# Performance work log

Measured on AMD Instinct MI355X. Metric: run time of the kernel, lower is better.

The kernel has to match this reference:

```python
import jax, jax.numpy as jnp
import numpy as np

N_NODES = 100000
N_RELS = 237
N_EDGES = 500000
D_IN = 128
D_HID = 128
D_OUT = 128


def setup_inputs() -> dict:
    key = jax.random.key(0)
    ks = jax.random.split(key, 13)
    src = jax.random.randint(ks[0], (N_EDGES,), 0, N_NODES, dtype=jnp.int32)
    dst = jax.random.randint(ks[1], (N_EDGES,), 0, N_NODES, dtype=jnp.int32)
    rel = jax.random.randint(ks[2], (N_EDGES,), 0, N_RELS, dtype=jnp.int32)
    triplets = jnp.stack([src, dst, rel], axis=1)  # [E, 3]
    s = 0.05
    return {
        "triplets": triplets,
        "ent_embed": jax.random.normal(ks[3], (N_NODES, D_IN), jnp.float32) * s,
        "rel_embed": jax.random.normal(ks[4], (N_RELS, D_IN), jnp.float32) * s,
        "W_ent": jax.random.normal(ks[5], (D_IN, D_HID), jnp.float32) * s,
        "b_ent": jnp.zeros((D_HID,), jnp.float32),
        "W_rel": jax.random.normal(ks[6], (D_IN, D_HID), jnp.float32) * s,
        "b_rel": jnp.zeros((D_HID,), jnp.float32),
        "W_ent2": jax.random.normal(ks[7], (3 * D_HID, D_OUT), jnp.float32) * s,
        "b_ent2": jnp.zeros((D_OUT,), jnp.float32),
        "a_w": jax.random.normal(ks[8], (D_OUT, 1), jnp.float32) * s,
        "a_b": jnp.zeros((1,), jnp.float32),
    }


def reference(triplets, ent_embed, rel_embed, W_ent, b_ent, W_rel, b_rel,
              W_ent2, b_ent2, a_w, a_b):
    src_i, dst_i, rel_i = triplets[:, 0], triplets[:, 1], triplets[:, 2]
    # embedding gathers
    src = ent_embed[src_i]          # [E, D_IN]
    dst = ent_embed[dst_i]          # [E, D_IN]
    rel = rel_embed[rel_i]          # [E, D_IN]
    # shared fc_ent projection on src and dst, fc_rel on rel
    src = src @ W_ent + b_ent       # [E, D_HID]
    dst = dst @ W_ent + b_ent
    rel = rel @ W_rel + b_rel
    # per-edge feature c = fc_ent2(cat([src, dst, rel]))
    c = jnp.concatenate([src, dst, rel], axis=1) @ W_ent2 + b_ent2  # [E, D_OUT]
    # unnormalized exp attention score (leaky_relu slope 0.01, torch default)
    b = jnp.exp(jax.nn.leaky_relu((c @ a_w + a_b)[:, 0], negative_slope=0.01))  # [E]
    # segment softmax over edges sharing a source node
    b_sum = jax.ops.segment_sum(b, src_i, num_segments=N_NODES)  # [N]
    alpha = b / b_sum[src_i]                                     # [E]
    # weighted neighbor aggregation per source node
    h = jax.ops.segment_sum(alpha[:, None] * c, src_i, num_segments=N_NODES)  # [N, D_OUT]
    return h
```

## Files before the change

### kernel.cpp

```cpp
#include <hip/hip_runtime.h>
#include <hip/hip_bf16.h>

#define N_NODES_C 100000
#define N_PAD_C   100096
#define N_RELS_C  237
#define N_EDGES_C 500000
#define D 128

#define NBLK_HIST 128
#define NBLK_REL  60
#define NBLK_GEMM 782
#define GEMM0     (NBLK_HIST + NBLK_REL)

typedef __attribute__((ext_vector_type(8))) short short8;
typedef __attribute__((ext_vector_type(4))) float f32x4;

__device__ __forceinline__ ushort f2bf(float x) {
    union { float f; uint u; } v; v.f = x;
    uint r = v.u + 0x7FFFu + ((v.u >> 16) & 1u);
    return (ushort)(r >> 16);
}
__device__ __forceinline__ float bf2f_hi(uint u) {
    union { uint u; float f; } v; v.u = u; return v.f;
}

__global__ void k_fuse_w(const float* __restrict__ W_ent, const float* __restrict__ W_rel,
                         const float* __restrict__ W_ent2,
                         const float* __restrict__ b_ent, const float* __restrict__ b_rel,
                         const float* __restrict__ b_ent2,
                         const float* __restrict__ a_w, const float* __restrict__ a_b,
                         float* __restrict__ WR, ushort* __restrict__ WfTb,
                         float* __restrict__ biasC, float* __restrict__ sConst,
                         int* __restrict__ deg) {
    int j = threadIdx.x;
    int k = blockIdx.x;
    int which = blockIdx.y;
    if (which == 0) {
        float acc = 0.f;
        for (int i = 0; i < D; ++i) acc += W_ent[k*D+i] * W_ent2[i*D+j];
        WfTb[j*D + k] = f2bf(acc);
    } else if (which == 1) {
        float acc = 0.f;
        for (int i = 0; i < D; ++i) acc += W_ent[k*D+i] * W_ent2[(D+i)*D+j];
        WfTb[(D+j)*D + k] = f2bf(acc);
    } else if (which == 2) {
        float acc = 0.f;
        for (int i = 0; i < D; ++i) acc += W_rel[k*D+i] * W_ent2[(2*D+i)*D+j];
        WR[k*D + j] = acc;
    } else if (k == 0) {
        __shared__ float red[128];
        float acc = b_ent2[j];
        for (int i = 0; i < D; ++i) {
            acc += b_ent[i] * (W_ent2[i*D+j] + W_ent2[(D+i)*D+j]);
            acc += b_rel[i] * W_ent2[(2*D+i)*D+j];
        }
        biasC[j] = acc;
        red[j] = acc * a_w[j];
        __syncthreads();
        for (int s = 64; s > 0; s >>= 1) { if (j < s) red[j] += red[j+s]; __syncthreads(); }
        if (j == 0) sConst[0] = red[0] + a_b[0];
    } else {
        int idx = (k - 1) * 128 + j;
        for (int i = idx; i < N_NODES_C; i += 127 * 128) deg[i] = 0;
    }
}

__global__ __launch_bounds__(512, 6) void k1_mega(const float* __restrict__ ent,
                                                  const ushort* __restrict__ WfTb,
                                                  const float* __restrict__ a_w,
                                                  const float* __restrict__ relE,
                                                  const float* __restrict__ WR,
                                                  const int* __restrict__ trip,
                                                  ushort* __restrict__ AnB,
                                                  ushort* __restrict__ BnB,
                                                  ushort* __restrict__ RmB,
                                                  float* __restrict__ sA,
                                                  float* __restrict__ sB,
                                                  float* __restrict__ sR,
                                                  int* __restrict__ deg,
                                                  int n_nodes) {
    __shared__ __align__(16) ushort wL[128*128];
    int tid = threadIdx.x;
    int blk = blockIdx.x;

    if (blk < NBLK_HIST) {
        for (int e = blk*512 + tid; e < N_EDGES_C; e += NBLK_HIST*512) {
            int s = trip[3*e];
            if ((unsigned)s < (unsigned)N_NODES_C) atomicAdd(&deg[s], 1);
        }
        return;
    }
    if (blk < GEMM0) {
        __shared__ float red[512];
        int sub = tid >> 7, j = tid & 127;
        int r = (blk - NBLK_HIST)*4 + sub;
        float acc = 0.f;
        if (r < N_RELS_C) {
            for (int k = 0; k < D; ++k) acc += relE[r*D+k] * WR[k*D+j];
            RmB[r*D + j] = f2bf(acc);
        }
        red[tid] = acc * a_w[j];
        __syncthreads();
        for (int s = 64; s > 0; s >>= 1) {
            if (j < s) red[sub*128 + j] += red[sub*128 + j + s];
            __syncthreads();
        }
        if (j == 0 && r < N_RELS_C) sR[r] = red[sub*128];
        return;
    }

    int tile = blk - GEMM0;
    int m0   = tile * 128;

    int wave = tid >> 6, lane = tid & 63;
    int q = lane >> 4, c = lane & 15;

    int row = m0 + wave*16 + c;
    float4 e0[4], e1[4];
#pragma unroll
    for (int chunk = 0; chunk < 4; ++chunk) {
        e0[chunk] = make_float4(0.f,0.f,0.f,0.f);
        e1[chunk] = e0[chunk];
    }
    if (row < n_nodes) {
        const float* ep = &ent[(size_t)row*D];
#pragma unroll
        for (int chunk = 0; chunk < 4; ++chunk) {
            int k16 = chunk*4 + q;
            e0[chunk] = *(const float4*)(ep + (k16 << 3));
            e1[chunk] = *(const float4*)(ep + (k16 << 3) + 4);
        }
    }

#pragma unroll
    for (int u = 0; u < 4; ++u) {
        int f = u*512 + tid;
        int r = f >> 4, k16 = f & 15;
        *(uint4*)&wL[r*128 + ((k16 ^ (r & 15)) << 3)] =
            *(const uint4*)&WfTb[r*128 + (k16 << 3)];
    }

    short8 a[4];
#pragma unroll
    for (int chunk = 0; chunk < 4; ++chunk) {
        short8 pk;
        pk[0]=(short)f2bf(e0[chunk].x); pk[1]=(short)f2bf(e0[chunk].y);
        pk[2]=(short)f2bf(e0[chunk].z); pk[3]=(short)f2bf(e0[chunk].w);
        pk[4]=(short)f2bf(e1[chunk].x); pk[5]=(short)f2bf(e1[chunk].y);
        pk[6]=(short)f2bf(e1[chunk].z); pk[7]=(short)f2bf(e1[chunk].w);
        a[chunk] = pk;
    }

    float aw[8];
#pragma unroll
    for (int nt = 0; nt < 8; ++nt) aw[nt] = a_w[nt*16 + c];

    __syncthreads();

    f32x4 acc[8];
#pragma unroll
    for (int nt = 0; nt < 8; ++nt) { f32x4 z = {0.f,0.f,0.f,0.f}; acc[nt] = z; }

#pragma unroll
    for (int chunk = 0; chunk < 4; ++chunk) {
        int k16 = chunk*4 + q;
#pragma unroll
        for (int nt = 0; nt < 8; ++nt) {
            short8 b = *(const short8*)&wL[(nt*16 + c)*128 + ((k16 ^ c) << 3)];
            acc[nt] = __builtin_amdgcn_mfma_f32_16x16x32_bf16(a[chunk], b, acc[nt], 0, 0, 0);
        }
    }

    __syncthreads();

#pragma unroll
    for (int u = 0; u < 4; ++u) {
        int f = u*512 + tid;
        int r = f >> 4, k16 = f & 15;
        *(uint4*)&wL[r*128 + ((k16 ^ (r & 15)) << 3)] =
            *(const uint4*)&WfTb[(128 + r)*128 + (k16 << 3)];
    }

#pragma unroll
    for (int reg = 0; reg < 4; ++reg) {
        int m = m0 + wave*16 + q*4 + reg;
        float pa = 0.f;
#pragma unroll
        for (int nt = 0; nt < 8; ++nt) pa += acc[nt][reg] * aw[nt];
#pragma unroll
        for (int msk = 1; msk < 16; msk <<= 1) pa += __shfl_xor(pa, msk);
        if (m < n_nodes) {
            if (c == 0) sA[m] = pa;
#pragma unroll
            for (int nt = 0; nt < 8; ++nt)
                AnB[(size_t)m*D + nt*16 + c] = f2bf(acc[nt][reg]);
        }
    }

    __syncthreads();

#pragma unroll
    for (int nt = 0; nt < 8; ++nt) { f32x4 z = {0.f,0.f,0.f,0.f}; acc[nt] = z; }

#pragma unroll
    for (int chunk = 0; chunk < 4; ++chunk) {
        int k16 = chunk*4 + q;
#pragma unroll
        for (int nt = 0; nt < 8; ++nt) {
            short8 b = *(const short8*)&wL[(nt*16 + c)*128 + ((k16 ^ c) << 3)];
            acc[nt] = __builtin_amdgcn_mfma_f32_16x16x32_bf16(a[chunk], b, acc[nt], 0, 0, 0);
        }
    }

#pragma unroll
    for (int reg = 0; reg < 4; ++reg) {
        int m = m0 + wave*16 + q*4 + reg;
        float pa = 0.f;
#pragma unroll
        for (int nt = 0; nt < 8; ++nt) pa += acc[nt][reg] * aw[nt];
#pragma unroll
        for (int msk = 1; msk < 16; msk <<= 1) pa += __shfl_xor(pa, msk);
        if (m < n_nodes) {
            if (c == 0) sB[m] = pa;
#pragma unroll
            for (int nt = 0; nt < 8; ++nt)
                BnB[(size_t)m*D + nt*16 + c] = f2bf(acc[nt][reg]);
        }
    }
}

__global__ void k_scan1(const int* __restrict__ deg, int* __restrict__ off,
                        int* __restrict__ bsum, int n) {
    __shared__ int s[1024];
    int i = blockIdx.x*1024 + threadIdx.x;
    int v = (i < n) ? deg[i] : 0;
    s[threadIdx.x] = v; __syncthreads();
    for (int d = 1; d < 1024; d <<= 1) {
        int t = (threadIdx.x >= d) ? s[threadIdx.x - d] : 0;
        __syncthreads();
        s[threadIdx.x] += t;
        __syncthreads();
    }
    if (i < n) off[i] = s[threadIdx.x] - v;
    if (threadIdx.x == 1023) bsum[blockIdx.x] = s[1023];
}

__global__ void k_scan23(int* __restrict__ off, int* __restrict__ cursor,
                         const int* __restrict__ bsum, int n, int nb, int total_edges) {
    __shared__ int s[128];
    int t = threadIdx.x;
    if (t < 128) s[t] = (t < nb) ? bsum[t] : 0;
    __syncthreads();
    for (int d = 1; d < 128; d <<= 1) {
        int u = (t < 128 && t >= d) ? s[t - d] : 0;
        __syncthreads();
        if (t < 128) s[t] += u;
        __syncthreads();
    }
    int add = (blockIdx.x > 0) ? s[blockIdx.x - 1] : 0;
    int i = blockIdx.x*1024 + t;
    if (i < n) {
        int o = off[i] + add;
        off[i] = o;
        cursor[i] = o;
    }
    if (i == 0) off[n] = total_edges;
}

__global__ void k_edge_b(const int* __restrict__ trip, const float* __restrict__ sB,
                         const float* __restrict__ sR, int* __restrict__ cursor,
                         uint2* __restrict__ kb, int n_edges) {
    int e = blockIdx.x*256 + threadIdx.x;
    if (e >= n_edges) return;
    int s = trip[3*e], d = trip[3*e+1], r = trip[3*e+2];
    if ((unsigned)s >= (unsigned)N_NODES_C || (unsigned)d >= (unsigned)N_NODES_C ||
        (unsigned)r >= (unsigned)N_RELS_C) return;
    float v = sB[d] + sR[r];
    int p = atomicAdd(&cursor[s], 1);
    kb[p] = make_uint2((uint)(d | (r << 20)), __float_as_uint(v));
}

__global__ void k_aggregate(const int* __restrict__ off, const uint2* __restrict__ kb,
                            const ushort* __restrict__ AnB, const ushort* __restrict__ BnB,
                            const ushort* __restrict__ RmB, const float* __restrict__ biasC,
                            const float* __restrict__ sA, const float* __restrict__ sConst,
                            float* __restrict__ h, int n_nodes) {
    int g = threadIdx.x >> 4, lane = threadIdx.x & 15;
    int n = blockIdx.x*16 + g;
    if (n >= n_nodes) return;
    int o0 = off[n], o1 = off[n+1];
    int c = lane*8;
    float* hp = &h[(size_t)n*D + c];
    if (o0 == o1) {
        *(float4*)hp     = make_float4(0.f,0.f,0.f,0.f);
        *(float4*)(hp+4) = make_float4(0.f,0.f,0.f,0.f);
        return;
    }
    float t = sA[n] + sConst[0];
    float num[8];
#pragma unroll
    for (int i = 0; i < 8; ++i) num[i] = 0.f;
    float den = 0.f;

    for (int p = o0; p < o1; p += 4) {
        uint2 kv[4]; uint4 gB[4], gR[4]; float vmask[4];
#pragma unroll
        for (int u = 0; u < 4; ++u) {
            int q = p + u;
            vmask[u] = (q < o1) ? 1.f : 0.f;
            int pc = (q < o1) ? q : (o1 - 1);
            kv[u] = kb[pc];
        }
#pragma unroll
        for (int u = 0; u < 4; ++u) {
            gB[u] = *(const uint4*)&BnB[(size_t)(kv[u].x & 0xFFFFF)*D + c];
            gR[u] = *(const uint4*)&RmB[(size_t)(kv[u].x >> 20)*D + c];
        }
#pragma unroll
        for (int u = 0; u < 4; ++u) {
            float logit = t + __uint_as_float(kv[u].y);
            float l = logit > 0.f ? logit : 0.01f*logit;
            float b = vmask[u] * expf(l);
            den += b;
            const uint* bu = (const uint*)&gB[u];
            const uint* ru = (const uint*)&gR[u];
#pragma unroll
            for (int i = 0; i < 4; ++i) {
                num[2*i]   += b * (bf2f_hi(bu[i] << 16)         + bf2f_hi(ru[i] << 16));
                num[2*i+1] += b * (bf2f_hi(bu[i] & 0xFFFF0000u) + bf2f_hi(ru[i] & 0xFFFF0000u));
            }
        }
    }

    float inv = 1.f / den;
    uint4 araw = *(const uint4*)&AnB[(size_t)n*D + c];
    const uint* au = (const uint*)&araw;
    float4 bc0 = *(const float4*)&biasC[c];
    float4 bc1 = *(const float4*)&biasC[c+4];
    float4 o0v, o1v;
    o0v.x = bf2f_hi(au[0] << 16)         + bc0.x + num[0]*inv;
    o0v.y = bf2f_hi(au[0] & 0xFFFF0000u) + bc0.y + num[1]*inv;
    o0v.z = bf2f_hi(au[1] << 16)         + bc0.z + num[2]*inv;
    o0v.w = bf2f_hi(au[1] & 0xFFFF0000u) + bc0.w + num[3]*inv;
    o1v.x = bf2f_hi(au[2] << 16)         + bc1.x + num[4]*inv;
    o1v.y = bf2f_hi(au[2] & 0xFFFF0000u) + bc1.y + num[5]*inv;
    o1v.z = bf2f_hi(au[3] << 16)         + bc1.z + num[6]*inv;
    o1v.w = bf2f_hi(au[3] & 0xFFFF0000u) + bc1.w + num[7]*inv;
    *(float4*)hp     = o0v;
    *(float4*)(hp+4) = o1v;
}

extern "C" void kernel_launch(void* const* d_in, const int* in_sizes, int n_in,
                              void* d_out, int out_size, void* d_ws, size_t ws_size,
                              hipStream_t stream) {
    const int*   trip   = (const int*)  d_in[0];
    const float* ent    = (const float*)d_in[1];
    const float* relE   = (const float*)d_in[2];
    const float* W_ent  = (const float*)d_in[3];
    const float* b_ent  = (const float*)d_in[4];
    const float* W_rel  = (const float*)d_in[5];
    const float* b_rel  = (const float*)d_in[6];
    const float* W_ent2 = (const float*)d_in[7];
    const float* b_ent2 = (const float*)d_in[8];
    const float* a_w    = (const float*)d_in[9];
    const float* a_b    = (const float*)d_in[10];
    float* h = (float*)d_out;

    char* ws = (char*)d_ws;
    size_t o = 0;
    auto alloc = [&](size_t bytes) { size_t p = o; o += (bytes + 255) & ~(size_t)255; return p; };
    float*  WR     = (float*) (ws + alloc(128*128*4));
    ushort* WfTb   = (ushort*)(ws + alloc(256*128*2));
    float*  biasC  = (float*) (ws + alloc(128*4));
    ushort* RmB    = (ushort*)(ws + alloc((size_t)N_RELS_C*128*2));
    float*  sR     = (float*) (ws + alloc(N_RELS_C*4));
    float*  sConst = (float*) (ws + alloc(4));
    float*  sA     = (float*) (ws + alloc((size_t)N_NODES_C*4));
    float*  sB     = (float*) (ws + alloc((size_t)N_NODES_C*4));
    int*    deg    = (int*)   (ws + alloc((size_t)N_NODES_C*4));
    int*    off    = (int*)   (ws + alloc(((size_t)N_NODES_C+1)*4));
    int*    cursor = (int*)   (ws + alloc((size_t)N_NODES_C*4));
    int*    bsum   = (int*)   (ws + alloc(128*4));
    uint2*  kb     = (uint2*) (ws + alloc((size_t)N_EDGES_C*8));
    ushort* BnB    = (ushort*)(ws + alloc((size_t)N_PAD_C*128*2));
    ushort* AnB    = (ushort*)(ws + alloc((size_t)N_PAD_C*128*2));

    k_fuse_w<<<dim3(128,4), 128, 0, stream>>>(W_ent, W_rel, W_ent2, b_ent, b_rel, b_ent2,
                                              a_w, a_b, WR, WfTb, biasC, sConst, deg);
    k1_mega<<<GEMM0 + NBLK_GEMM, 512, 0, stream>>>(
        ent, WfTb, a_w, relE, WR, trip, AnB, BnB, RmB, sA, sB, sR, deg, N_NODES_C);
    int nb = (N_NODES_C + 1023)/1024;
    k_scan1<<<nb, 1024, 0, stream>>>(deg, off, bsum, N_NODES_C);
    k_scan23<<<nb, 1024, 0, stream>>>(off, cursor, bsum, N_NODES_C, nb, N_EDGES_C);
    k_edge_b<<<(N_EDGES_C+255)/256, 256, 0, stream>>>(trip, sB, sR, cursor, kb, N_EDGES_C);
    k_aggregate<<<(N_NODES_C+15)/16, 256, 0, stream>>>(off, kb, AnB, BnB, RmB, biasC,
                                                       sA, sConst, h, N_NODES_C);
}
```

Baseline: 235.7 us.

## Fuse pipeline into one cooperative persistent kernel with grid syncs

Replaces the six-kernel launch sequence with a single cooperative kernel that runs the weight fusion, histogram, GEMMs, scan, edge bucketing and aggregation as phases separated by grid-wide syncs. It also splits each GEMM tile into two blocks, one per weight half, so each block does one MFMA pass, doubling the GEMM block count. The goal is to remove launch gaps and inter-kernel tail effects. The cost is grid-sync overhead, and the grid is capped at 1024 resident blocks, so later phases get less parallelism. The old multi-kernel path is kept as a fallback.

```diff
diff --git a/kernel.cpp b/kernel.cpp
--- a/kernel.cpp
+++ b/kernel.cpp
@@ -1,5 +1,8 @@
 #include <hip/hip_runtime.h>
+#include <hip/hip_cooperative_groups.h>
 #include <hip/hip_bf16.h>
+
+namespace cg = cooperative_groups;
 
 #define N_NODES_C 100000
 #define N_PAD_C   100096
@@ -9,8 +12,11 @@
 
 #define NBLK_HIST 128
 #define NBLK_REL  60
-#define NBLK_GEMM 782
+#define NBLK_GEMM 1568
 #define GEMM0     (NBLK_HIST + NBLK_REL)
+#define NBLK_P1   (GEMM0 + NBLK_GEMM)
+
+#define NTHR   512
 
 typedef __attribute__((ext_vector_type(8))) short short8;
 typedef __attribute__((ext_vector_type(4))) float f32x4;
@@ -22,6 +28,303 @@
 }
 __device__ __forceinline__ float bf2f_hi(uint u) {
     union { uint u; float f; } v; v.u = u; return v.f;
+}
+
+__global__ __launch_bounds__(NTHR, 4) void k_mega(
+    const int* __restrict__ trip, const float* __restrict__ ent,
+    const float* __restrict__ relE,
+    const float* __restrict__ W_ent, const float* __restrict__ b_ent,
+    const float* __restrict__ W_rel, const float* __restrict__ b_rel,
+    const float* __restrict__ W_ent2, const float* __restrict__ b_ent2,
+    const float* __restrict__ a_w, const float* __restrict__ a_b,
+    float* __restrict__ h,
+    float* __restrict__ WR, ushort* __restrict__ WfTb,
+    float* __restrict__ biasC, float* __restrict__ sConst,
+    ushort* __restrict__ RmB, float* __restrict__ sR,
+    float* __restrict__ sA, float* __restrict__ sB,
+    int* __restrict__ deg, int* __restrict__ off, int* __restrict__ cursor,
+    int* __restrict__ bsum, uint2* __restrict__ kb,
+    ushort* __restrict__ AnB, ushort* __restrict__ BnB)
+{
+    __shared__ __align__(16) union {
+        ushort wL[128*128];
+        float  red[512];
+        int    scan[1024];
+    } sm;
+
+    cg::grid_group gridg = cg::this_grid();
+    int tid = threadIdx.x, blk = blockIdx.x;
+    int nblk = gridDim.x;
+
+    {
+        int f = blk*NTHR + tid;
+        if (blk < 96) {
+            int which = f >> 14;
+            int r = f & 16383;
+            int k = r >> 7, j = r & 127;
+            float acc = 0.f;
+            if (which == 0) {
+                for (int i = 0; i < D; ++i) acc += W_ent[k*D+i] * W_ent2[i*D+j];
+                WfTb[j*D + k] = f2bf(acc);
+            } else if (which == 1) {
+                for (int i = 0; i < D; ++i) acc += W_ent[k*D+i] * W_ent2[(D+i)*D+j];
+                WfTb[(D+j)*D + k] = f2bf(acc);
+            } else {
+                for (int i = 0; i < D; ++i) acc += W_rel[k*D+i] * W_ent2[(2*D+i)*D+j];
+                WR[k*D + j] = acc;
+            }
+        } else if (blk == 96) {
+            int j = tid;
+            if (j < 128) {
+                float acc = b_ent2[j];
+                for (int i = 0; i < D; ++i) {
+                    acc += b_ent[i] * (W_ent2[i*D+j] + W_ent2[(D+i)*D+j]);
+                    acc += b_rel[i] * W_ent2[(2*D+i)*D+j];
+                }
+                biasC[j] = acc;
+                sm.red[j] = acc * a_w[j];
+            }
+            __syncthreads();
+            for (int s = 64; s > 0; s >>= 1) {
+                if (j < s) sm.red[j] += sm.red[j+s];
+                __syncthreads();
+            }
+            if (j == 0) sConst[0] = sm.red[0] + a_b[0];
+        } else {
+            int idx = (blk - 97)*NTHR + tid;
+            int stride = (nblk - 97)*NTHR;
+            for (int i = idx; i < N_NODES_C; i += stride) deg[i] = 0;
+        }
+    }
+    gridg.sync();
+
+    for (int vb = blk; vb < NBLK_P1; vb += nblk) {
+        if (vb < NBLK_HIST) {
+            for (int e = vb*NTHR + tid; e < N_EDGES_C; e += NBLK_HIST*NTHR) {
+                int s = trip[3*e];
+                if ((unsigned)s < (unsigned)N_NODES_C) atomicAdd(&deg[s], 1);
+            }
+        } else if (vb < GEMM0) {
+            __syncthreads();
+            int sub = tid >> 7, j = tid & 127;
+            int r = (vb - NBLK_HIST)*4 + sub;
+            float acc = 0.f;
+            if (r < N_RELS_C) {
+                for (int k = 0; k < D; ++k) acc += relE[r*D+k] * WR[k*D+j];
+                RmB[r*D + j] = f2bf(acc);
+            }
+            sm.red[tid] = acc * a_w[j];
+            __syncthreads();
+            for (int s = 64; s > 0; s >>= 1) {
+                if (j < s) sm.red[sub*128 + j] += sm.red[sub*128 + j + s];
+                __syncthreads();
+            }
+            if (j == 0 && r < N_RELS_C) sR[r] = sm.red[sub*128];
+        } else {
+            int g    = vb - GEMM0;
+            int half = (g >> 3) & 1;
+            int tile = ((g >> 4) << 3) + (g & 7);
+            int m0   = tile * 128;
+
+            int wave = tid >> 6, lane = tid & 63;
+            int q = lane >> 4, c = lane & 15;
+
+            int row = m0 + wave*16 + c;
+            float4 e0[4], e1[4];
+#pragma unroll
+            for (int chunk = 0; chunk < 4; ++chunk) {
+                e0[chunk] = make_float4(0.f,0.f,0.f,0.f);
+                e1[chunk] = e0[chunk];
+            }
+            if (row < N_NODES_C) {
+                const float* ep = &ent[(size_t)row*D];
+#pragma unroll
+                for (int chunk = 0; chunk < 4; ++chunk) {
+                    int k16 = chunk*4 + q;
+                    e0[chunk] = *(const float4*)(ep + (k16 << 3));
+                    e1[chunk] = *(const float4*)(ep + (k16 << 3) + 4);
+                }
+            }
+
+            __syncthreads();
+
+#pragma unroll
+            for (int u = 0; u < 4; ++u) {
+                int f = u*NTHR + tid;
+                int r = f >> 4, k16 = f & 15;
+                *(uint4*)&sm.wL[r*128 + ((k16 ^ (r & 15)) << 3)] =
+                    *(const uint4*)&WfTb[(half*128 + r)*128 + (k16 << 3)];
+            }
+
+            short8 a[4];
+#pragma unroll
+            for (int chunk = 0; chunk < 4; ++chunk) {
+                short8 pk;
+                pk[0]=(short)f2bf(e0[chunk].x); pk[1]=(short)f2bf(e0[chunk].y);
+                pk[2]=(short)f2bf(e0[chunk].z); pk[3]=(short)f2bf(e0[chunk].w);
+                pk[4]=(short)f2bf(e1[chunk].x); pk[5]=(short)f2bf(e1[chunk].y);
+                pk[6]=(short)f2bf(e1[chunk].z); pk[7]=(short)f2bf(e1[chunk].w);
+                a[chunk] = pk;
+            }
+            __syncthreads();
+
+            f32x4 acc[8];
+#pragma unroll
+            for (int nt = 0; nt < 8; ++nt) { f32x4 z = {0.f,0.f,0.f,0.f}; acc[nt] = z; }
+
+#pragma unroll
+            for (int chunk = 0; chunk < 4; ++chunk) {
+                int k16 = chunk*4 + q;
+#pragma unroll
+                for (int nt = 0; nt < 8; ++nt) {
+                    short8 b = *(const short8*)&sm.wL[(nt*16 + c)*128 + ((k16 ^ c) << 3)];
+                    acc[nt] = __builtin_amdgcn_mfma_f32_16x16x32_bf16(a[chunk], b, acc[nt], 0, 0, 0);
+                }
+            }
+
+            float aw[8];
+#pragma unroll
+            for (int nt = 0; nt < 8; ++nt) aw[nt] = a_w[nt*16 + c];
+
+            ushort* out  = half ? BnB : AnB;
+            float*  sOut = half ? sB  : sA;
+
+#pragma unroll
+            for (int reg = 0; reg < 4; ++reg) {
+                int m = m0 + wave*16 + q*4 + reg;
+                float pa = 0.f;
+#pragma unroll
+                for (int nt = 0; nt < 8; ++nt) pa += acc[nt][reg] * aw[nt];
+#pragma unroll
+                for (int msk = 1; msk < 16; msk <<= 1) pa += __shfl_xor(pa, msk);
+                if (m < N_NODES_C) {
+                    if (c == 0) sOut[m] = pa;
+#pragma unroll
+                    for (int nt = 0; nt < 8; ++nt)
+                        out[(size_t)m*D + nt*16 + c] = f2bf(acc[nt][reg]);
+                }
+            }
+        }
+    }
+    gridg.sync();
+
+    for (int vb = blk; vb < 98; vb += nblk) {
+        __syncthreads();
+        int i0 = vb*1024 + 2*tid;
+        int d0 = (i0     < N_NODES_C) ? deg[i0]   : 0;
+        int d1 = (i0 + 1 < N_NODES_C) ? deg[i0+1] : 0;
+        sm.scan[tid] = d0 + d1;
+        __syncthreads();
+        for (int d = 1; d < 512; d <<= 1) {
+            int t2 = (tid >= d) ? sm.scan[tid-d] : 0;
+            __syncthreads();
+            sm.scan[tid] += t2;
+            __syncthreads();
+        }
+        int excl = sm.scan[tid] - (d0 + d1);
+        if (i0     < N_NODES_C) off[i0]   = excl;
+        if (i0 + 1 < N_NODES_C) off[i0+1] = excl + d0;
+        if (tid == 511) bsum[vb] = sm.scan[511];
+    }
+    gridg.sync();
+
+    for (int vb = blk; vb < 98; vb += nblk) {
+        __syncthreads();
+        if (tid < 128) sm.scan[tid] = (tid < 98) ? bsum[tid] : 0;
+        __syncthreads();
+        for (int d = 1; d < 128; d <<= 1) {
+            int u = (tid < 128 && tid >= d) ? sm.scan[tid-d] : 0;
+            __syncthreads();
+            if (tid < 128) sm.scan[tid] += u;
+            __syncthreads();
+        }
+        int add = (vb > 0) ? sm.scan[vb-1] : 0;
+        int i0 = vb*1024 + 2*tid;
+        if (i0     < N_NODES_C) { int o = off[i0]   + add; off[i0]   = o; cursor[i0]   = o; }
+        if (i0 + 1 < N_NODES_C) { int o = off[i0+1] + add; off[i0+1] = o; cursor[i0+1] = o; }
+    }
+    if (blk == 0 && tid == 0) off[N_NODES_C] = N_EDGES_C;
+    gridg.sync();
+
+    for (int e = blk*NTHR + tid; e < N_EDGES_C; e += nblk*NTHR) {
+        int s = trip[3*e], d = trip[3*e+1], r = trip[3*e+2];
+        if ((unsigned)s < (unsigned)N_NODES_C && (unsigned)d < (unsigned)N_NODES_C &&
+            (unsigned)r < (unsigned)N_RELS_C) {
+            float v = sB[d] + sR[r];
+            int p = atomicAdd(&cursor[s], 1);
+            kb[p] = make_uint2((uint)(d | (r << 20)), __float_as_uint(v));
+        }
+    }
+    gridg.sync();
+
+    {
+        int gg = tid >> 4, lane = tid & 15;
+        for (int base = blk*32; base < N_NODES_C; base += nblk*32) {
+            int n = base + gg;
+            if (n < N_NODES_C) {
+                int o0 = off[n], o1 = off[n+1];
+                int c = lane*8;
+                float* hp = &h[(size_t)n*D + c];
+                if (o0 == o1) {
+                    *(float4*)hp     = make_float4(0.f,0.f,0.f,0.f);
+                    *(float4*)(hp+4) = make_float4(0.f,0.f,0.f,0.f);
+                } else {
+                    float t = sA[n] + sConst[0];
+                    float num[8];
+#pragma unroll
+                    for (int i = 0; i < 8; ++i) num[i] = 0.f;
+                    float den = 0.f;
+
+                    for (int p = o0; p < o1; p += 4) {
+                        uint2 kv[4]; uint4 gB[4], gR[4]; float vmask[4];
+#pragma unroll
+                        for (int u = 0; u < 4; ++u) {
+                            int qq = p + u;
+                            vmask[u] = (qq < o1) ? 1.f : 0.f;
+                            int pc = (qq < o1) ? qq : (o1 - 1);
+                            kv[u] = kb[pc];
+                        }
+#pragma unroll
+                        for (int u = 0; u < 4; ++u) {
+                            gB[u] = *(const uint4*)&BnB[(size_t)(kv[u].x & 0xFFFFF)*D + c];
+                            gR[u] = *(const uint4*)&RmB[(size_t)(kv[u].x >> 20)*D + c];
+                        }
+#pragma unroll
+                        for (int u = 0; u < 4; ++u) {
+                            float logit = t + __uint_as_float(kv[u].y);
+                            float l = logit > 0.f ? logit : 0.01f*logit;
+                            float b = vmask[u] * expf(l);
+                            den += b;
+                            const uint* bu = (const uint*)&gB[u];
+                            const uint* ru = (const uint*)&gR[u];
+#pragma unroll
+                            for (int i = 0; i < 4; ++i) {
+                                num[2*i]   += b * (bf2f_hi(bu[i] << 16)         + bf2f_hi(ru[i] << 16));
+                                num[2*i+1] += b * (bf2f_hi(bu[i] & 0xFFFF0000u) + bf2f_hi(ru[i] & 0xFFFF0000u));
+                            }
+                        }
+                    }
+
+                    float inv = 1.f / den;
+                    uint4 araw = *(const uint4*)&AnB[(size_t)n*D + c];
+                    const uint* au = (const uint*)&araw;
+                    float4 bc0 = *(const float4*)&biasC[c];
+                    float4 bc1 = *(const float4*)&biasC[c+4];
+                    float4 o0v, o1v;
+                    o0v.x = bf2f_hi(au[0] << 16)         + bc0.x + num[0]*inv;
+                    o0v.y = bf2f_hi(au[0] & 0xFFFF0000u) + bc0.y + num[1]*inv;
+                    o0v.z = bf2f_hi(au[1] << 16)         + bc0.z + num[2]*inv;
+                    o0v.w = bf2f_hi(au[1] & 0xFFFF0000u) + bc0.w + num[3]*inv;
+                    o1v.x = bf2f_hi(au[2] << 16)         + bc1.x + num[4]*inv;
+                    o1v.y = bf2f_hi(au[2] & 0xFFFF0000u) + bc1.y + num[5]*inv;
+                    o1v.z = bf2f_hi(au[3] << 16)         + bc1.z + num[6]*inv;
+                    o1v.w = bf2f_hi(au[3] & 0xFFFF0000u) + bc1.w + num[7]*inv;
+                    *(float4*)hp     = o0v;
+                    *(float4*)(hp+4) = o1v;
+                }
+            }
+        }
+    }
 }
 
 __global__ void k_fuse_w(const float* __restrict__ W_ent, const float* __restrict__ W_rel,
@@ -109,7 +412,9 @@
         return;
     }
 
-    int tile = blk - GEMM0;
+    int g    = blk - GEMM0;
+    int half = (g >> 3) & 1;
+    int tile = ((g >> 4) << 3) + (g & 7);
     int m0   = tile * 128;
 
     int wave = tid >> 6, lane = tid & 63;
@@ -137,7 +442,7 @@
         int f = u*512 + tid;
         int r = f >> 4, k16 = f & 15;
         *(uint4*)&wL[r*128 + ((k16 ^ (r & 15)) << 3)] =
-            *(const uint4*)&WfTb[r*128 + (k16 << 3)];
+            *(const uint4*)&WfTb[(half*128 + r)*128 + (k16 << 3)];
     }
 
     short8 a[4];
@@ -150,11 +455,6 @@
         pk[6]=(short)f2bf(e1[chunk].z); pk[7]=(short)f2bf(e1[chunk].w);
         a[chunk] = pk;
     }
-
-    float aw[8];
-#pragma unroll
-    for (int nt = 0; nt < 8; ++nt) aw[nt] = a_w[nt*16 + c];
-
     __syncthreads();
 
     f32x4 acc[8];
@@ -171,15 +471,12 @@
         }
     }
 
-    __syncthreads();
-
-#pragma unroll
-    for (int u = 0; u < 4; ++u) {
-        int f = u*512 + tid;
-        int r = f >> 4, k16 = f & 15;
-        *(uint4*)&wL[r*128 + ((k16 ^ (r & 15)) << 3)] =
-            *(const uint4*)&WfTb[(128 + r)*128 + (k16 << 3)];
-    }
+    float aw[8];
+#pragma unroll
+    for (int nt = 0; nt < 8; ++nt) aw[nt] = a_w[nt*16 + c];
+
+    ushort* out  = half ? BnB : AnB;
+    float*  sOut = half ? sB  : sA;
 
 #pragma unroll
     for (int reg = 0; reg < 4; ++reg) {
@@ -190,41 +487,10 @@
 #pragma unroll
         for (int msk = 1; msk < 16; msk <<= 1) pa += __shfl_xor(pa, msk);
         if (m < n_nodes) {
-            if (c == 0) sA[m] = pa;
+            if (c == 0) sOut[m] = pa;
 #pragma unroll
             for (int nt = 0; nt < 8; ++nt)
-                AnB[(size_t)m*D + nt*16 + c] = f2bf(acc[nt][reg]);
-        }
-    }
-
-    __syncthreads();
-
-#pragma unroll
-    for (int nt = 0; nt < 8; ++nt) { f32x4 z = {0.f,0.f,0.f,0.f}; acc[nt] = z; }
-
-#pragma unroll
-    for (int chunk = 0; chunk < 4; ++chunk) {
-        int k16 = chunk*4 + q;
-#pragma unroll
-        for (int nt = 0; nt < 8; ++nt) {
-            short8 b = *(const short8*)&wL[(nt*16 + c)*128 + ((k16 ^ c) << 3)];
-            acc[nt] = __builtin_amdgcn_mfma_f32_16x16x32_bf16(a[chunk], b, acc[nt], 0, 0, 0);
-        }
-    }
-
-#pragma unroll
-    for (int reg = 0; reg < 4; ++reg) {
-        int m = m0 + wave*16 + q*4 + reg;
-        float pa = 0.f;
-#pragma unroll
-        for (int nt = 0; nt < 8; ++nt) pa += acc[nt][reg] * aw[nt];
-#pragma unroll
-        for (int msk = 1; msk < 16; msk <<= 1) pa += __shfl_xor(pa, msk);
-        if (m < n_nodes) {
-            if (c == 0) sB[m] = pa;
-#pragma unroll
-            for (int nt = 0; nt < 8; ++nt)
-                BnB[(size_t)m*D + nt*16 + c] = f2bf(acc[nt][reg]);
+                out[(size_t)m*D + nt*16 + c] = f2bf(acc[nt][reg]);
         }
     }
 }
@@ -385,14 +651,53 @@
     ushort* BnB    = (ushort*)(ws + alloc((size_t)N_PAD_C*128*2));
     ushort* AnB    = (ushort*)(ws + alloc((size_t)N_PAD_C*128*2));
 
-    k_fuse_w<<<dim3(128,4), 128, 0, stream>>>(W_ent, W_rel, W_ent2, b_ent, b_rel, b_ent2,
-                                              a_w, a_b, WR, WfTb, biasC, sConst, deg);
-    k1_mega<<<GEMM0 + NBLK_GEMM, 512, 0, stream>>>(
-        ent, WfTb, a_w, relE, WR, trip, AnB, BnB, RmB, sA, sB, sR, deg, N_NODES_C);
-    int nb = (N_NODES_C + 1023)/1024;
-    k_scan1<<<nb, 1024, 0, stream>>>(deg, off, bsum, N_NODES_C);
-    k_scan23<<<nb, 1024, 0, stream>>>(off, cursor, bsum, N_NODES_C, nb, N_EDGES_C);
-    k_edge_b<<<(N_EDGES_C+255)/256, 256, 0, stream>>>(trip, sB, sR, cursor, kb, N_EDGES_C);
-    k_aggregate<<<(N_NODES_C+15)/16, 256, 0, stream>>>(off, kb, AnB, BnB, RmB, biasC,
-                                                       sA, sConst, h, N_NODES_C);
-}
+    static int coop_grid = -2;
+    if (coop_grid == -2) {
+        int maxb = 0;
+        hipError_t e1 = hipOccupancyMaxActiveBlocksPerMultiprocessor(
+            &maxb, (const void*)k_mega, NTHR, 0);
+        int cus = 0, dev = 0;
+        hipDeviceProp_t prop;
+        if (hipGetDevice(&dev) == hipSuccess &&
+            hipGetDeviceProperties(&prop, dev) == hipSuccess)
+            cus = prop.multiProcessorCount;
+        if (e1 == hipSuccess && maxb > 0 && cus > 0) {
+            long g = (long)maxb * (long)cus;
+            if (g > 1024) g = 1024;
+            coop_grid = (g >= 98) ? (int)g : -1;
+        } else {
+            coop_grid = -1;
+        }
+    }
+
+    bool launched = false;
+    if (coop_grid > 0) {
+        void* args[] = {
+            (void*)&trip, (void*)&ent, (void*)&relE,
+            (void*)&W_ent, (void*)&b_ent, (void*)&W_rel, (void*)&b_rel,
+            (void*)&W_ent2, (void*)&b_ent2, (void*)&a_w, (void*)&a_b,
+            (void*)&h,
+            (void*)&WR, (void*)&WfTb, (void*)&biasC, (void*)&sConst,
+            (void*)&RmB, (void*)&sR, (void*)&sA, (void*)&sB,
+            (void*)&deg, (void*)&off, (void*)&cursor, (void*)&bsum,
+            (void*)&kb, (void*)&AnB, (void*)&BnB
+        };
+        launched = (hipLaunchCooperativeKernel((const void*)k_mega,
+                        dim3(coop_grid), dim3(NTHR), args, 0, stream) == hipSuccess);
+        if (!launched) coop_grid = -1;
+    }
+
+    if (!launched) {
+        k_fuse_w<<<dim3(128,4), 128, 0, stream>>>(W_ent, W_rel, W_ent2, b_ent, b_rel,
+                                                  b_ent2, a_w, a_b, WR, WfTb, biasC,
+                                                  sConst, deg);
+        k1_mega<<<GEMM0 + NBLK_GEMM, 512, 0, stream>>>(
+            ent, WfTb, a_w, relE, WR, trip, AnB, BnB, RmB, sA, sB, sR, deg, N_NODES_C);
+        int nb = (N_NODES_C + 1023)/1024;
+        k_scan1<<<nb, 1024, 0, stream>>>(deg, off, bsum, N_NODES_C);
+        k_scan23<<<nb, 1024, 0, stream>>>(off, cursor, bsum, N_NODES_C, nb, N_EDGES_C);
+        k_edge_b<<<(N_EDGES_C+255)/256, 256, 0, stream>>>(trip, sB, sR, cursor, kb, N_EDGES_C);
+        k_aggregate<<<(N_NODES_C+15)/16, 256, 0, stream>>>(off, kb, AnB, BnB, RmB, biasC,
+                                                           sA, sConst, h, N_NODES_C);
+    }
+}
```

New measurement: 401.9 us. 70.5% more time.
